# Kernel tuning notes

Measured on AMD Instinct MI355X. Metric: run time of the kernel, lower is better.

Reference implementation:

```python
import math
import jax, jax.numpy as jnp
import numpy as np

INP_MODES = [4, 8, 8, 4]   # prod = 1024 = in_features
OUT_MODES = [8, 8, 8, 8]   # prod = 4096 = out_features
TT_RANKS = [1, 8, 8, 8, 1]
IN_FEATURES = 1024
OUT_FEATURES = 4096
BATCH = 8192
D = len(INP_MODES)


def setup_inputs() -> dict:
    key = jax.random.key(0)
    ks = jax.random.split(key, D + 2)
    inp = {"x": jax.random.normal(ks[0], (BATCH, IN_FEATURES), dtype=jnp.float32)}
    for i in range(D):
        # xavier_normal per the module's reset_parameters
        fan_in = TT_RANKS[i] * INP_MODES[i]
        fan_out = TT_RANKS[i + 1] * OUT_MODES[i]
        std = math.sqrt(2.0 / (fan_in + fan_out))
        shape = (TT_RANKS[i] * OUT_MODES[i], TT_RANKS[i + 1] * INP_MODES[i])
        inp[f"core{i}"] = std * jax.random.normal(ks[i + 1], shape, dtype=jnp.float32)
    bound = 1.0 / math.sqrt(IN_FEATURES)
    inp["bias"] = jax.random.uniform(ks[D + 1], (OUT_FEATURES,), dtype=jnp.float32,
                                     minval=-bound, maxval=bound)
    return inp


def _tt_forward(x, cores, bias):
    # x: [B, in_features]. Sequentially contract input modes against TT cores.
    # Invariant after step i: h has shape (B, M=prod(m_0..m_i), r_{i+1}, N=prod(n_{i+1}..))
    B = x.shape[0]
    h = x.reshape(B, 1, 1, IN_FEATURES)
    for i, c in enumerate(cores):
        r, m, q, n = TT_RANKS[i], OUT_MODES[i], TT_RANKS[i + 1], INP_MODES[i]
        c4 = c.reshape(r, m, q, n)          # (r_i, m_i, r_{i+1}, n_i)
        M = h.shape[1]
        h = h.reshape(B, M, r, n, -1)       # split current input mode n_i
        # contract rank r_i and input mode n_i; produce out mode m_i (s) and next rank q
        h = jnp.einsum('bmrnp,rsqn->bmsqp', h, c4)
        h = h.reshape(B, M * m, q, -1)
    y = h.reshape(B, OUT_FEATURES) + bias
    return y


def reference(x, core0, core1, core2, core3, bias):
    return _tt_forward(x, [core0, core1, core2, core3], bias)
```

## Files before the change

kernel.cpp:

```cpp
#include <hip/hip_runtime.h>
#include <hip/hip_bf16.h>

typedef __bf16 bf16x4 __attribute__((ext_vector_type(4)));
typedef __bf16 bf16x8 __attribute__((ext_vector_type(8)));
typedef float  f32x4  __attribute__((ext_vector_type(4)));
typedef float  f32x16 __attribute__((ext_vector_type(16)));

#define MFMA32(a,b,c) __builtin_amdgcn_mfma_f32_32x32x16_bf16((a),(b),(c),0,0,0)

#define BAR_LDS() asm volatile("s_waitcnt lgkmcnt(0)\n\ts_barrier" ::: "memory")


__global__ __launch_bounds__(256) void prep_kernel(
    const float* __restrict__ c0, const float* __restrict__ c1,
    const float* __restrict__ c2, const float* __restrict__ c3,
    __bf16* __restrict__ ws)
{
    const int gid = blockIdx.x * 256 + threadIdx.x;
    if (gid < 16384) {
      const int j   = gid & 7,        c32 = (gid >> 3) & 31;
      const int hh  = (gid >> 8) & 1, kt  = (gid >> 9) & 1;
      const int m0  = (gid >> 10) & 7, rt = (gid >> 13) & 1;
      const int row = rt * 32 + c32, m1 = row >> 3, r2 = row & 7;
      const int n0  = kt * 2 + hh, n1 = j;
      float s = 0.f;
      #pragma unroll
      for (int r1 = 0; r1 < 8; ++r1)
        s += c0[m0 * 32 + r1 * 4 + n0] * c1[(r1 * 8 + m1) * 64 + r2 * 8 + n1];
      ws[gid] = (__bf16)s;
    } else {
      const int idx = gid - 16384;
      const int j   = idx & 7,        c32 = (idx >> 3) & 31;
      const int hh  = (idx >> 8) & 1, kt  = (idx >> 9) & 15;
      const int rt  = (idx >> 13) & 1;
      const int row = rt * 32 + c32, m2 = row >> 3, m3 = row & 7;
      const int k   = (kt * 2 + hh) * 8 + j;
      const int n2  = k >> 5, n3 = (k >> 3) & 3, r2 = k & 7;
      float s = 0.f;
      #pragma unroll
      for (int r3 = 0; r3 < 8; ++r3)
        s += c2[(r2 * 8 + m2) * 64 + r3 * 8 + n2] * c3[(r3 * 8 + m3) * 4 + n3];
      ws[gid] = (__bf16)s;
    }
}

__global__ __launch_bounds__(256, 3) void tt_kernel(
    const float* __restrict__ x, const float* __restrict__ bias,
    const __bf16* __restrict__ ws, float* __restrict__ y)
{
    __shared__ __align__(16) __bf16 hb[16384];
    __shared__ __align__(16) __bf16 xt[2048];

    const int tid  = threadIdx.x;
    const int wid  = tid >> 6;
    const int lane = tid & 63;
    const int hh   = lane >> 5;
    const int c32  = lane & 31;
    const int rt   = wid & 1;
    const int ct   = wid >> 1;

    const __bf16* ws01 = ws;
    const __bf16* ws23 = ws + 16384;
    const int b0 = blockIdx.x * 2;

#define LOAD_W01(qc, DST) do { \
    _Pragma("unroll") \
    for (int m0h = 0; m0h < 4; ++m0h) \
      _Pragma("unroll") \
      for (int kt = 0; kt < 2; ++kt) \
        DST[m0h][kt] = *(const bf16x8*)&ws01[rt * 8192 + ((qc) * 4 + m0h) * 1024 \
                                             + kt * 512 + hh * 256 + c32 * 8]; \
  } while (0)

#define STAGE_A(WQ) do { \
    _Pragma("unroll") \
    for (int m0h = 0; m0h < 4; ++m0h) { \
      f32x16 acc_ = {}; \
      acc_ = MFMA32(WQ[m0h][0], xf[0], acc_); \
      acc_ = MFMA32(WQ[m0h][1], xf[1], acc_); \
      _Pragma("unroll") \
      for (int p = 0; p < 4; ++p) { \
        bf16x4 o_; \
        _Pragma("unroll") \
        for (int i = 0; i < 4; ++i) o_[i] = (__bf16)acc_[p * 4 + i]; \
        const int cl_ = ct * 32 + m0h * 8 + rt * 4 + p; \
        *(bf16x4*)&hb[cl_ * 256 + ((c32 ^ (cl_ & 31)) << 3) + hh * 4] = o_; \
      } \
    } \
  } while (0)

#define STAGE_B_EPI(qc) do { \
    const __bf16* brow_ = &hb[(ct * 32 + c32) * 256]; \
    const __bf16* wrow_ = ws23 + rt * 8192 + hh * 256 + c32 * 8; \
    f32x16 a2a_ = {}, a2b_ = {}; \
    _Pragma("unroll") \
    for (int kt = 0; kt < 16; kt += 2) { \
      const bf16x8 w0_ = *(const bf16x8*)&wrow_[kt * 512]; \
      const bf16x8 w1_ = *(const bf16x8*)&wrow_[(kt + 1) * 512]; \
      const bf16x8 b0_ = *(const bf16x8*)&brow_[((kt * 2 + hh) ^ c32) << 3]; \
      const bf16x8 b1_ = *(const bf16x8*)&brow_[((kt * 2 + 2 + hh) ^ c32) << 3]; \
      a2a_ = MFMA32(b0_, w0_, a2a_); \
      a2b_ = MFMA32(b1_, w1_, a2b_); \
    } \
    const size_t yb_ = (size_t)(b0 + ct) * 4096 + (qc) * 2048 + rt * 32 + c32; \
    const int bb_ = (qc) * 2048 + rt * 32 + c32; \
    _Pragma("unroll") \
    for (int p = 0; p < 4; ++p) \
      _Pragma("unroll") \
      for (int i = 0; i < 4; ++i) \
        y[yb_ + p * 512 + (hh * 4 + i) * 64] = \
            (a2a_[p * 4 + i] + a2b_[p * 4 + i]) + bias[bb_ + p * 512 + (hh * 4 + i) * 64]; \
  } while (0)

    const int bsel = tid >> 7, xcol = tid & 31, k0q = (tid >> 5) & 3;
    float xv[8];
    {
      const float* xp = x + (size_t)(b0 + bsel) * 1024 + xcol;
      #pragma unroll
      for (int j = 0; j < 8; ++j) xv[j] = xp[(k0q * 8 + j) * 32];
    }
    bf16x8 w01q[4][2];
    LOAD_W01(0, w01q);
    {
      bf16x8 v;
      #pragma unroll
      for (int j = 0; j < 8; ++j) v[j] = (__bf16)xv[j];
      *(bf16x8*)&xt[(bsel * 32 + xcol) * 32 + ((k0q ^ (xcol & 3)) << 3)] = v;
    }
    BAR_LDS();

    bf16x8 xf[2];
    #pragma unroll
    for (int kt = 0; kt < 2; ++kt)
      xf[kt] = *(const bf16x8*)
        &xt[(ct * 32 + c32) * 32 + (((kt * 2 + hh) ^ (c32 & 3)) << 3)];
    STAGE_A(w01q);
    bf16x8 w01n[4][2];
    LOAD_W01(1, w01n);
    BAR_LDS();
    STAGE_B_EPI(0);
    BAR_LDS();

    STAGE_A(w01n);
    BAR_LDS();
    STAGE_B_EPI(1);

#undef LOAD_W01
#undef STAGE_A
#undef STAGE_B_EPI
}

extern "C" void kernel_launch(void* const* d_in, const int* in_sizes, int n_in,
                              void* d_out, int out_size, void* d_ws, size_t ws_size,
                              hipStream_t stream) {
    const float* x    = (const float*)d_in[0];
    const float* c0   = (const float*)d_in[1];
    const float* c1   = (const float*)d_in[2];
    const float* c2   = (const float*)d_in[3];
    const float* c3   = (const float*)d_in[4];
    const float* bias = (const float*)d_in[5];
    float* yout = (float*)d_out;
    __bf16* ws = (__bf16*)d_ws;

    prep_kernel<<<128, 256, 0, stream>>>(c0, c1, c2, c3, ws);
    tt_kernel<<<4096, 256, 0, stream>>>(x, bias, ws, yout);
}
```

Baseline: 191.3 us.

## Make TT kernel persistent over four batch pairs with prefetched x and resident weights

Each block now handles four pairs of batch rows in a loop instead of one, which cuts the grid to a quarter. The fused first-stage weights are loaded into registers once per block, and the next iteration's x tile is prefetched into registers while the current one is computed. This amortises weight loads and launch overhead and overlaps global x reads with MFMA work. The cost is more registers per thread, a higher occupancy hint in launch bounds, and fewer blocks to hide latency.

Measured after the change: 328.8 us. 71.9% more time.

```diff
diff --git a/kernel.cpp b/kernel.cpp
--- a/kernel.cpp
+++ b/kernel.cpp
@@ -44,7 +44,9 @@
     }
 }
 
-__global__ __launch_bounds__(256, 3) void tt_kernel(
+#define TT_ITERS 4
+
+__global__ __launch_bounds__(256, 4) void tt_kernel(
     const float* __restrict__ x, const float* __restrict__ bias,
     const __bf16* __restrict__ ws, float* __restrict__ y)
 {
@@ -61,23 +63,36 @@
 
     const __bf16* ws01 = ws;
     const __bf16* ws23 = ws + 16384;
-    const int b0 = blockIdx.x * 2;
 
-#define LOAD_W01(qc, DST) do { \
+    const int bsel = tid >> 7, xcol = tid & 31, k0q = (tid >> 5) & 3;
+    const int xtoff = (bsel * 32 + xcol) * 32 + ((k0q ^ (xcol & 3)) << 3);
+
+#define LOAD_X(itn) do { \
+    const float* xp_ = x + (size_t)((blockIdx.x * TT_ITERS + (itn)) * 2 + bsel) * 1024 + xcol; \
     _Pragma("unroll") \
-    for (int m0h = 0; m0h < 4; ++m0h) \
-      _Pragma("unroll") \
-      for (int kt = 0; kt < 2; ++kt) \
-        DST[m0h][kt] = *(const bf16x8*)&ws01[rt * 8192 + ((qc) * 4 + m0h) * 1024 \
-                                             + kt * 512 + hh * 256 + c32 * 8]; \
+    for (int j = 0; j < 8; ++j) xv[j] = xp_[(k0q * 8 + j) * 32]; \
   } while (0)
 
-#define STAGE_A(WQ) do { \
+#define WRITE_XT() do { \
+    bf16x8 v_; \
+    _Pragma("unroll") \
+    for (int j = 0; j < 8; ++j) v_[j] = (__bf16)xv[j]; \
+    *(bf16x8*)&xt[xtoff] = v_; \
+  } while (0)
+
+#define READ_XF() do { \
+    _Pragma("unroll") \
+    for (int kt = 0; kt < 2; ++kt) \
+      xf[kt] = *(const bf16x8*) \
+        &xt[(ct * 32 + c32) * 32 + (((kt * 2 + hh) ^ (c32 & 3)) << 3)]; \
+  } while (0)
+
+#define STAGE_A(qc) do { \
     _Pragma("unroll") \
     for (int m0h = 0; m0h < 4; ++m0h) { \
       f32x16 acc_ = {}; \
-      acc_ = MFMA32(WQ[m0h][0], xf[0], acc_); \
-      acc_ = MFMA32(WQ[m0h][1], xf[1], acc_); \
+      acc_ = MFMA32(w01f[(qc) * 4 + m0h][0], xf[0], acc_); \
+      acc_ = MFMA32(w01f[(qc) * 4 + m0h][1], xf[1], acc_); \
       _Pragma("unroll") \
       for (int p = 0; p < 4; ++p) { \
         bf16x4 o_; \
@@ -89,7 +104,7 @@
     } \
   } while (0)
 
-#define STAGE_B_EPI(qc) do { \
+#define STAGE_B_EPI(qc, itp) do { \
     const __bf16* brow_ = &hb[(ct * 32 + c32) * 256]; \
     const __bf16* wrow_ = ws23 + rt * 8192 + hh * 256 + c32 * 8; \
     f32x16 a2a_ = {}, a2b_ = {}; \
@@ -102,7 +117,8 @@
       a2a_ = MFMA32(b0_, w0_, a2a_); \
       a2b_ = MFMA32(b1_, w1_, a2b_); \
     } \
-    const size_t yb_ = (size_t)(b0 + ct) * 4096 + (qc) * 2048 + rt * 32 + c32; \
+    const size_t yb_ = (size_t)((blockIdx.x * TT_ITERS + (itp)) * 2 + ct) * 4096 \
+                       + (qc) * 2048 + rt * 32 + c32; \
     const int bb_ = (qc) * 2048 + rt * 32 + c32; \
     _Pragma("unroll") \
     for (int p = 0; p < 4; ++p) \
@@ -112,40 +128,39 @@
             (a2a_[p * 4 + i] + a2b_[p * 4 + i]) + bias[bb_ + p * 512 + (hh * 4 + i) * 64]; \
   } while (0)
 
-    const int bsel = tid >> 7, xcol = tid & 31, k0q = (tid >> 5) & 3;
     float xv[8];
-    {
-      const float* xp = x + (size_t)(b0 + bsel) * 1024 + xcol;
+    LOAD_X(0);
+
+    bf16x8 w01f[8][2];
+    #pragma unroll
+    for (int m0 = 0; m0 < 8; ++m0)
       #pragma unroll
-      for (int j = 0; j < 8; ++j) xv[j] = xp[(k0q * 8 + j) * 32];
-    }
-    bf16x8 w01q[4][2];
-    LOAD_W01(0, w01q);
-    {
-      bf16x8 v;
-      #pragma unroll
-      for (int j = 0; j < 8; ++j) v[j] = (__bf16)xv[j];
-      *(bf16x8*)&xt[(bsel * 32 + xcol) * 32 + ((k0q ^ (xcol & 3)) << 3)] = v;
-    }
+      for (int kt = 0; kt < 2; ++kt)
+        w01f[m0][kt] = *(const bf16x8*)&ws01[rt * 8192 + m0 * 1024
+                                             + kt * 512 + hh * 256 + c32 * 8];
+
+    WRITE_XT();
     BAR_LDS();
 
     bf16x8 xf[2];
-    #pragma unroll
-    for (int kt = 0; kt < 2; ++kt)
-      xf[kt] = *(const bf16x8*)
-        &xt[(ct * 32 + c32) * 32 + (((kt * 2 + hh) ^ (c32 & 3)) << 3)];
-    STAGE_A(w01q);
-    bf16x8 w01n[4][2];
-    LOAD_W01(1, w01n);
-    BAR_LDS();
-    STAGE_B_EPI(0);
-    BAR_LDS();
+    #pragma unroll 1
+    for (int it = 0; it < TT_ITERS; ++it) {
+      READ_XF();
+      if (it + 1 < TT_ITERS) LOAD_X(it + 1);
+      STAGE_A(0);
+      BAR_LDS();
+      STAGE_B_EPI(0, it);
+      if (it + 1 < TT_ITERS) WRITE_XT();
+      BAR_LDS();
+      STAGE_A(1);
+      BAR_LDS();
+      STAGE_B_EPI(1, it);
+      BAR_LDS();
+    }
 
-    STAGE_A(w01n);
-    BAR_LDS();
-    STAGE_B_EPI(1);
-
-#undef LOAD_W01
+#undef LOAD_X
+#undef WRITE_XT
+#undef READ_XF
 #undef STAGE_A
 #undef STAGE_B_EPI
 }
@@ -163,5 +178,5 @@
     __bf16* ws = (__bf16*)d_ws;
 
     prep_kernel<<<128, 256, 0, stream>>>(c0, c1, c2, c3, ws);
-    tt_kernel<<<4096, 256, 0, stream>>>(x, bias, ws, yout);
+    tt_kernel<<<1024, 256, 0, stream>>>(x, bias, ws, yout);
 }
```
